# Performance work log

Measured on AMD Instinct MI355X. Metric: run time of the kernel, lower is better.

The kernel has to match this reference:

```python
import jax, jax.numpy as jnp
import numpy as np

B, C, O, H, W, K = 8, 64, 64, 96, 96, 3
PAD = 1


def setup_inputs() -> dict:
    key = jax.random.key(0)
    ks = jax.random.split(key, 5)
    x = jax.random.normal(ks[0], (B, C, H, W), jnp.float32)
    # small offset weights so sampled offsets stay O(1) pixel, like a trained net
    offset_w = jax.random.normal(ks[1], (2 * K * K, C, K, K), jnp.float32) * 0.01
    offset_b = jnp.zeros((2 * K * K,), jnp.float32)
    conv_w = jax.random.normal(ks[2], (O, C, K, K), jnp.float32) * (1.0 / np.sqrt(C * K * K))
    conv_b = jax.random.normal(ks[3], (O,), jnp.float32) * 0.01
    return {"x": x, "offset_w": offset_w, "offset_b": offset_b,
            "conv_w": conv_w, "conv_b": conv_b}


def _conv2d(x, w, b, pad):
    out = jax.lax.conv_general_dilated(
        x, w, window_strides=(1, 1), padding=[(pad, pad), (pad, pad)],
        dimension_numbers=("NCHW", "OIHW", "NCHW"))
    return out + b[None, :, None, None]


def _gather(x_flat, yi, xi):
    # x_flat: [B, C, H*W]; yi, xi: [B, K2, H, W] int32 sample indices
    valid = (yi >= 0) & (yi < H) & (xi >= 0) & (xi < W)
    idx = jnp.clip(yi, 0, H - 1) * W + jnp.clip(xi, 0, W - 1)
    idx_f = idx.reshape(idx.shape[0], -1)  # [B, K2*H*W]
    vals = jax.vmap(lambda xf, i: xf[:, i])(x_flat, idx_f)  # [B, C, K2*H*W]
    vals = vals.reshape(x_flat.shape[0], x_flat.shape[1], *idx.shape[1:])
    return vals * valid[:, None].astype(vals.dtype)  # zero padding outside


def _deform_conv2d(x, offset, w, b, pad):
    # Faithful to torchvision.ops.deform_conv2d (v1, 1 offset group, stride 1)
    K2 = K * K
    off = offset.reshape(offset.shape[0], K2, 2, H, W)
    dy, dx = off[:, :, 0], off[:, :, 1]  # (dy, dx) per kernel tap, torchvision order
    ky = jnp.repeat(jnp.arange(K), K).astype(x.dtype)  # row index i of tap k=i*K+j
    kx = jnp.tile(jnp.arange(K), K).astype(x.dtype)    # col index j
    # fractional sample positions [B, K2, H, W]
    py = jnp.arange(H, dtype=x.dtype)[None, None, :, None] - pad + ky[None, :, None, None] + dy
    px = jnp.arange(W, dtype=x.dtype)[None, None, None, :] - pad + kx[None, :, None, None] + dx
    y0 = jnp.floor(py)
    x0 = jnp.floor(px)
    wy = (py - y0)[:, None]  # broadcast over channels
    wx = (px - x0)[:, None]
    y0i = y0.astype(jnp.int32)
    x0i = x0.astype(jnp.int32)
    x_flat = x.reshape(x.shape[0], x.shape[1], H * W)
    g00 = _gather(x_flat, y0i, x0i)
    g01 = _gather(x_flat, y0i, x0i + 1)
    g10 = _gather(x_flat, y0i + 1, x0i)
    g11 = _gather(x_flat, y0i + 1, x0i + 1)
    # bilinear interp -> sampled patches [B, C, K2, H, W]
    sampled = (g00 * (1 - wy) * (1 - wx) + g01 * (1 - wy) * wx
               + g10 * wy * (1 - wx) + g11 * wy * wx)
    out = jnp.einsum("bckhw,ock->bohw", sampled, w.reshape(w.shape[0], w.shape[1], K2))
    return out + b[None, :, None, None]


def reference(x, offset_w, offset_b, conv_w, conv_b):
    offset = _conv2d(x, offset_w, offset_b, PAD)  # [B, 18, H, W]
    return _deform_conv2d(x, offset, conv_w, conv_b, PAD)
```

## Files before the change

kernel.cpp:

```cpp
#include <hip/hip_runtime.h>

#define Bb 8
#define Cc 64
#define Oo 64
#define Hh 96
#define Ww 96
#define HW 9216
#define NOFF 18

typedef __bf16 bf16_t;
typedef __bf16 bf16x2 __attribute__((ext_vector_type(2)));
typedef __bf16 bf16x8 __attribute__((ext_vector_type(8)));
typedef float  f32x4  __attribute__((ext_vector_type(4)));

#define OFFS_SZ (Bb*NOFF*HW)
#define XT_SZ   (Bb*HW*Cc)
#define WTPD_SZ (18*4*64*8)
#define WTPO_SZ (18*2*64*8)

__global__ void xpose_kernel(const float* __restrict__ x, bf16_t* __restrict__ xt) {
    __shared__ float tile[64][65];
    int bid  = blockIdx.x;
    int b    = bid / 144;
    int t0   = (bid % 144) * 64;
    int lane = threadIdx.x & 63;
    int sub  = threadIdx.x >> 6;
    const float* xb = x + (size_t)b * Cc * HW;
    #pragma unroll
    for (int i = 0; i < 16; ++i) {
        int c = sub * 16 + i;
        tile[c][lane] = xb[c * HW + t0 + lane];
    }
    __syncthreads();
    bf16_t* xtb = xt + ((size_t)b * HW + t0) * Cc;
    int half = lane >> 5, cpair = lane & 31;
    #pragma unroll
    for (int i = 0; i < 8; ++i) {
        int hw = sub * 16 + half * 8 + i;
        bf16x2 v;
        v[0] = (bf16_t)tile[cpair * 2][hw];
        v[1] = (bf16_t)tile[cpair * 2 + 1][hw];
        *(bf16x2*)&xtb[hw * Cc + cpair * 2] = v;
    }
}

__global__ void prep_w(const float* __restrict__ cw, const float* __restrict__ ow,
                       bf16_t* __restrict__ wtpd, bf16_t* __restrict__ wtpo) {
    if (blockIdx.x < 18) {
        int n = blockIdx.x * 256 + threadIdx.x;
        int t = n >> 8; int rem = n & 255; int mt = rem >> 6; int l = rem & 63;
        int o = mt * 16 + (l & 15);
        int kbase = t * 32 + ((l >> 4) & 3) * 8;
        bf16x8 v;
        #pragma unroll
        for (int j = 0; j < 8; ++j) {
            int kidx = kbase + j; int k = kidx >> 6; int c = kidx & 63;
            v[j] = (bf16_t)cw[(o * 64 + c) * 9 + k];
        }
        *(bf16x8*)&wtpd[n * 8] = v;
    } else {
        int n = (blockIdx.x - 18) * 256 + threadIdx.x;
        int t = n >> 7; int rem = n & 127; int mt = rem >> 6; int l = rem & 63;
        int oc = mt * 16 + (l & 15);
        int kbase = t * 32 + ((l >> 4) & 3) * 8;
        bf16x8 v;
        #pragma unroll
        for (int j = 0; j < 8; ++j) {
            int kidx = kbase + j; int k = kidx >> 6; int c = kidx & 63;
            v[j] = (oc < NOFF) ? (bf16_t)ow[(oc * 64 + c) * 9 + k] : (bf16_t)0.f;
        }
        *(bf16x8*)&wtpo[n * 8] = v;
    }
}


__global__ __launch_bounds__(256, 4) void offconv_mfma(const bf16_t* __restrict__ xt,
        const bf16_t* __restrict__ wtpo, const float* __restrict__ ob,
        float* __restrict__ offs) {
    __shared__ bf16_t Sb[4][16 * 72];
    int bid = blockIdx.x;
    int b = bid & 7, hw0 = (bid >> 3) * 64;
    int tid = threadIdx.x, lane = tid & 63, q = tid >> 6;
    int cg = lane & 7, prow = lane >> 3;
    int cb8 = cg * 8;
    int ph[2], pw[2];
    #pragma unroll
    for (int i = 0; i < 2; ++i) {
        int hw = hw0 + q * 16 + i * 8 + prow;
        ph[i] = hw / 96; pw[i] = hw % 96;
    }
    f32x4 acc[2];
    #pragma unroll
    for (int mt = 0; mt < 2; ++mt)
        #pragma unroll
        for (int r = 0; r < 4; ++r) {
            int oc = mt * 16 + ((lane >> 4) & 3) * 4 + r;
            acc[mt][r] = (oc < NOFF) ? ob[oc] : 0.f;
        }
    bf16_t* myS = &Sb[q][0];
    int bbase = b * HW;

    bf16x8 g[2];
    auto issue = [&](int k, bf16x8 (&gg)[2]) {
        const int ky = k / 3, kx = k % 3;
        #pragma unroll
        for (int i = 0; i < 2; ++i) {
            int y = ph[i] - 1 + ky, x = pw[i] - 1 + kx;
            bool valid = (y >= 0) && (y < Hh) && (x >= 0) && (x < Ww);
            bf16x8 v;
            #pragma unroll
            for (int j = 0; j < 8; ++j) v[j] = (bf16_t)0.f;
            if (valid) v = *(const bf16x8*)(xt + ((bbase + y * Ww + x) * Cc + cb8));
            gg[i] = v;
        }
    };
    issue(0, g);
    #pragma unroll
    for (int k = 0; k < 9; ++k) {
        #pragma unroll
        for (int i = 0; i < 2; ++i)
            *(bf16x8*)&myS[(i * 8 + prow) * 72 + cb8] = g[i];
        if (k < 8) issue(k + 1, g);
        #pragma unroll
        for (int s = 0; s < 2; ++s) {
            bf16x8 bfrag = *(bf16x8*)&myS[(lane & 15) * 72 + s * 32 + ((lane >> 4) & 3) * 8];
            int t = k * 2 + s;
            #pragma unroll
            for (int mt = 0; mt < 2; ++mt) {
                bf16x8 afrag = *(const bf16x8*)&wtpo[((t * 2 + mt) * 64 + lane) * 8];
                acc[mt] = __builtin_amdgcn_mfma_f32_16x16x32_bf16(afrag, bfrag, acc[mt], 0, 0, 0);
            }
        }
    }
    #pragma unroll
    for (int mt = 0; mt < 2; ++mt)
        #pragma unroll
        for (int r = 0; r < 4; ++r) {
            int oc = mt * 16 + ((lane >> 4) & 3) * 4 + r;
            if (oc < NOFF)
                offs[(b * NOFF + oc) * HW + hw0 + q * 16 + (lane & 15)] = acc[mt][r];
        }
}

__global__ __launch_bounds__(256, 4) void deform_mfma(const bf16_t* __restrict__ xt,
        const float* __restrict__ offs, const bf16_t* __restrict__ wtpd,
        const float* __restrict__ cb, float* __restrict__ out) {
    __shared__ float offbuf[64 * 20];
    __shared__ bf16_t Sa[4][16 * 72];
    int bid = blockIdx.x;
    int b = bid & 7, hw0 = (bid >> 3) * 64;
    int tid = threadIdx.x, lane = tid & 63, q = tid >> 6;
    {
        int pix = tid & 63, oc0 = tid >> 6;
        #pragma unroll
        for (int r = 0; r < 5; ++r) {
            int oc = oc0 + r * 4;
            if (oc < NOFF)
                offbuf[pix * 20 + oc] = offs[(b * NOFF + oc) * HW + hw0 + pix];
        }
    }
    __syncthreads();
    int cg = lane & 7, prow = lane >> 3;
    int cb8 = cg * 8;
    int pl[2], ph[2], pw[2];
    #pragma unroll
    for (int i = 0; i < 2; ++i) {
        pl[i] = q * 16 + i * 8 + prow;
        int hw = hw0 + pl[i];
        ph[i] = hw / 96; pw[i] = hw % 96;
    }
    f32x4 acc[4];
    #pragma unroll
    for (int mt = 0; mt < 4; ++mt)
        #pragma unroll
        for (int r = 0; r < 4; ++r)
            acc[mt][r] = cb[mt * 16 + ((lane >> 4) & 3) * 4 + r];
    bf16_t* myS = &Sa[q][0];
    int bbase = b * HW;

    bf16x8 g[2][4];
    float w4[2][4];
    auto issue = [&](int k, bf16x8 (&gg)[2][4], float (&ww)[2][4]) {
        const int ky = k / 3, kx = k % 3;
        #pragma unroll
        for (int i = 0; i < 2; ++i) {
            float2 od = *(float2*)&offbuf[pl[i] * 20 + 2 * k];
            float py = (float)(ph[i] - 1 + ky) + od.x;
            float px = (float)(pw[i] - 1 + kx) + od.y;
            float fy = floorf(py), fx = floorf(px);
            float wy = py - fy, wx = px - fx;
            int y0 = (int)fy, x0 = (int)fx;
            int y1 = y0 + 1, x1 = x0 + 1;
            bool vy0 = (unsigned)y0 < (unsigned)Hh, vy1 = (unsigned)y1 < (unsigned)Hh;
            bool vx0 = (unsigned)x0 < (unsigned)Ww, vx1 = (unsigned)x1 < (unsigned)Ww;
            int y0c = min(max(y0, 0), Hh - 1), y1c = min(max(y1, 0), Hh - 1);
            int x0c = min(max(x0, 0), Ww - 1), x1c = min(max(x1, 0), Ww - 1);
            ww[i][0] = (vy0 && vx0) ? (1.f - wy) * (1.f - wx) : 0.f;
            ww[i][1] = (vy0 && vx1) ? (1.f - wy) * wx : 0.f;
            ww[i][2] = (vy1 && vx0) ? wy * (1.f - wx) : 0.f;
            ww[i][3] = (vy1 && vx1) ? wy * wx : 0.f;
            int r0 = (bbase + y0c * Ww) * Cc, r1 = (bbase + y1c * Ww) * Cc;
            gg[i][0] = *(const bf16x8*)(xt + r0 + x0c * Cc + cb8);
            gg[i][1] = *(const bf16x8*)(xt + r0 + x1c * Cc + cb8);
            gg[i][2] = *(const bf16x8*)(xt + r1 + x0c * Cc + cb8);
            gg[i][3] = *(const bf16x8*)(xt + r1 + x1c * Cc + cb8);
        }
    };
    issue(0, g, w4);
    #pragma unroll
    for (int k = 0; k < 9; ++k) {
        #pragma unroll
        for (int i = 0; i < 2; ++i) {
            bf16x8 v;
            #pragma unroll
            for (int j = 0; j < 8; ++j) {
                float s = (float)g[i][0][j] * w4[i][0] + (float)g[i][1][j] * w4[i][1]
                        + (float)g[i][2][j] * w4[i][2] + (float)g[i][3][j] * w4[i][3];
                v[j] = (bf16_t)s;
            }
            *(bf16x8*)&myS[(i * 8 + prow) * 72 + cb8] = v;
        }
        if (k < 8) issue(k + 1, g, w4);
        #pragma unroll
        for (int s = 0; s < 2; ++s) {
            bf16x8 bfrag = *(bf16x8*)&myS[(lane & 15) * 72 + s * 32 + ((lane >> 4) & 3) * 8];
            int t = k * 2 + s;
            #pragma unroll
            for (int mt = 0; mt < 4; ++mt) {
                bf16x8 afrag = *(const bf16x8*)&wtpd[((t * 4 + mt) * 64 + lane) * 8];
                acc[mt] = __builtin_amdgcn_mfma_f32_16x16x32_bf16(afrag, bfrag, acc[mt], 0, 0, 0);
            }
        }
    }
    #pragma unroll
    for (int mt = 0; mt < 4; ++mt)
        #pragma unroll
        for (int r = 0; r < 4; ++r) {
            int o = mt * 16 + ((lane >> 4) & 3) * 4 + r;
            out[(b * Oo + o) * HW + hw0 + q * 16 + (lane & 15)] = acc[mt][r];
        }
}

extern "C" void kernel_launch(void* const* d_in, const int* in_sizes, int n_in,
                              void* d_out, int out_size, void* d_ws, size_t ws_size,
                              hipStream_t stream) {
    const float* x  = (const float*)d_in[0];
    const float* ow = (const float*)d_in[1];
    const float* ob = (const float*)d_in[2];
    const float* cw = (const float*)d_in[3];
    const float* cb = (const float*)d_in[4];
    float* out = (float*)d_out;

    float*  offs = (float*)d_ws;
    bf16_t* xt   = (bf16_t*)(offs + OFFS_SZ);
    bf16_t* wtpd = xt + XT_SZ;
    bf16_t* wtpo = wtpd + WTPD_SZ;

    xpose_kernel<<<1152, 256, 0, stream>>>(x, xt);
    prep_w      <<<27,   256, 0, stream>>>(cw, ow, wtpd, wtpo);
    offconv_mfma<<<1152, 256, 0, stream>>>(xt, wtpo, ob, offs);
    deform_mfma <<<1152, 256, 0, stream>>>(xt, offs, wtpd, cb, out);
}
```

Baseline: 119.9 us.

## Fuse offset conv into deform kernel and merge transpose with weight prep

Computes the offset convolution inside the deformable conv kernel and writes offsets straight to shared memory. This removes the global offset buffer round trip and one launch. The transpose and weight-prep kernels are also merged into one launch with block-index dispatch. In exchange, each block now runs both phases back to back, with a __syncthreads between them and higher per-block register and latency pressure.

Measured after the change: 113.9 us. 5.0% less time.

```diff
diff --git a/kernel.cpp b/kernel.cpp
--- a/kernel.cpp
+++ b/kernel.cpp
@@ -13,41 +13,39 @@
 typedef __bf16 bf16x8 __attribute__((ext_vector_type(8)));
 typedef float  f32x4  __attribute__((ext_vector_type(4)));
 
-#define OFFS_SZ (Bb*NOFF*HW)
 #define XT_SZ   (Bb*HW*Cc)
 #define WTPD_SZ (18*4*64*8)
 #define WTPO_SZ (18*2*64*8)
 
-__global__ void xpose_kernel(const float* __restrict__ x, bf16_t* __restrict__ xt) {
+__global__ void xpose_prep(const float* __restrict__ x, const float* __restrict__ cw,
+                           const float* __restrict__ ow, bf16_t* __restrict__ xt,
+                           bf16_t* __restrict__ wtpd, bf16_t* __restrict__ wtpo) {
     __shared__ float tile[64][65];
-    int bid  = blockIdx.x;
-    int b    = bid / 144;
-    int t0   = (bid % 144) * 64;
-    int lane = threadIdx.x & 63;
-    int sub  = threadIdx.x >> 6;
-    const float* xb = x + (size_t)b * Cc * HW;
-    #pragma unroll
-    for (int i = 0; i < 16; ++i) {
-        int c = sub * 16 + i;
-        tile[c][lane] = xb[c * HW + t0 + lane];
-    }
-    __syncthreads();
-    bf16_t* xtb = xt + ((size_t)b * HW + t0) * Cc;
-    int half = lane >> 5, cpair = lane & 31;
-    #pragma unroll
-    for (int i = 0; i < 8; ++i) {
-        int hw = sub * 16 + half * 8 + i;
-        bf16x2 v;
-        v[0] = (bf16_t)tile[cpair * 2][hw];
-        v[1] = (bf16_t)tile[cpair * 2 + 1][hw];
-        *(bf16x2*)&xtb[hw * Cc + cpair * 2] = v;
-    }
-}
-
-__global__ void prep_w(const float* __restrict__ cw, const float* __restrict__ ow,
-                       bf16_t* __restrict__ wtpd, bf16_t* __restrict__ wtpo) {
-    if (blockIdx.x < 18) {
-        int n = blockIdx.x * 256 + threadIdx.x;
+    int bid = blockIdx.x;
+    if (bid < 1152) {
+        int b    = bid / 144;
+        int t0   = (bid % 144) * 64;
+        int lane = threadIdx.x & 63;
+        int sub  = threadIdx.x >> 6;
+        const float* xb = x + (size_t)b * Cc * HW;
+        #pragma unroll
+        for (int i = 0; i < 16; ++i) {
+            int c = sub * 16 + i;
+            tile[c][lane] = xb[c * HW + t0 + lane];
+        }
+        __syncthreads();
+        bf16_t* xtb = xt + ((size_t)b * HW + t0) * Cc;
+        int half = lane >> 5, cpair = lane & 31;
+        #pragma unroll
+        for (int i = 0; i < 8; ++i) {
+            int hw = sub * 16 + half * 8 + i;
+            bf16x2 v;
+            v[0] = (bf16_t)tile[cpair * 2][hw];
+            v[1] = (bf16_t)tile[cpair * 2 + 1][hw];
+            *(bf16x2*)&xtb[hw * Cc + cpair * 2] = v;
+        }
+    } else if (bid < 1170) {
+        int n = (bid - 1152) * 256 + threadIdx.x;
         int t = n >> 8; int rem = n & 255; int mt = rem >> 6; int l = rem & 63;
         int o = mt * 16 + (l & 15);
         int kbase = t * 32 + ((l >> 4) & 3) * 8;
@@ -59,7 +57,7 @@
         }
         *(bf16x8*)&wtpd[n * 8] = v;
     } else {
-        int n = (blockIdx.x - 18) * 256 + threadIdx.x;
+        int n = (bid - 1170) * 256 + threadIdx.x;
         int t = n >> 7; int rem = n & 127; int mt = rem >> 6; int l = rem & 63;
         int oc = mt * 16 + (l & 15);
         int kbase = t * 32 + ((l >> 4) & 3) * 8;
@@ -73,95 +71,21 @@
     }
 }
 
-
-__global__ __launch_bounds__(256, 4) void offconv_mfma(const bf16_t* __restrict__ xt,
-        const bf16_t* __restrict__ wtpo, const float* __restrict__ ob,
-        float* __restrict__ offs) {
-    __shared__ bf16_t Sb[4][16 * 72];
+__global__ __launch_bounds__(256, 4) void fused_dcn(const bf16_t* __restrict__ xt,
+        const bf16_t* __restrict__ wtpo, const bf16_t* __restrict__ wtpd,
+        const float* __restrict__ ob, const float* __restrict__ cb,
+        float* __restrict__ out) {
+    __shared__ float offbuf[64 * 20];
+    __shared__ bf16_t Sa[4][16 * 72];
+
     int bid = blockIdx.x;
     int b = bid & 7, hw0 = (bid >> 3) * 64;
     int tid = threadIdx.x, lane = tid & 63, q = tid >> 6;
     int cg = lane & 7, prow = lane >> 3;
     int cb8 = cg * 8;
-    int ph[2], pw[2];
-    #pragma unroll
-    for (int i = 0; i < 2; ++i) {
-        int hw = hw0 + q * 16 + i * 8 + prow;
-        ph[i] = hw / 96; pw[i] = hw % 96;
-    }
-    f32x4 acc[2];
-    #pragma unroll
-    for (int mt = 0; mt < 2; ++mt)
-        #pragma unroll
-        for (int r = 0; r < 4; ++r) {
-            int oc = mt * 16 + ((lane >> 4) & 3) * 4 + r;
-            acc[mt][r] = (oc < NOFF) ? ob[oc] : 0.f;
-        }
-    bf16_t* myS = &Sb[q][0];
+    bf16_t* myS = &Sa[q][0];
     int bbase = b * HW;
 
-    bf16x8 g[2];
-    auto issue = [&](int k, bf16x8 (&gg)[2]) {
-        const int ky = k / 3, kx = k % 3;
-        #pragma unroll
-        for (int i = 0; i < 2; ++i) {
-            int y = ph[i] - 1 + ky, x = pw[i] - 1 + kx;
-            bool valid = (y >= 0) && (y < Hh) && (x >= 0) && (x < Ww);
-            bf16x8 v;
-            #pragma unroll
-            for (int j = 0; j < 8; ++j) v[j] = (bf16_t)0.f;
-            if (valid) v = *(const bf16x8*)(xt + ((bbase + y * Ww + x) * Cc + cb8));
-            gg[i] = v;
-        }
-    };
-    issue(0, g);
-    #pragma unroll
-    for (int k = 0; k < 9; ++k) {
-        #pragma unroll
-        for (int i = 0; i < 2; ++i)
-            *(bf16x8*)&myS[(i * 8 + prow) * 72 + cb8] = g[i];
-        if (k < 8) issue(k + 1, g);
-        #pragma unroll
-        for (int s = 0; s < 2; ++s) {
-            bf16x8 bfrag = *(bf16x8*)&myS[(lane & 15) * 72 + s * 32 + ((lane >> 4) & 3) * 8];
-            int t = k * 2 + s;
-            #pragma unroll
-            for (int mt = 0; mt < 2; ++mt) {
-                bf16x8 afrag = *(const bf16x8*)&wtpo[((t * 2 + mt) * 64 + lane) * 8];
-                acc[mt] = __builtin_amdgcn_mfma_f32_16x16x32_bf16(afrag, bfrag, acc[mt], 0, 0, 0);
-            }
-        }
-    }
-    #pragma unroll
-    for (int mt = 0; mt < 2; ++mt)
-        #pragma unroll
-        for (int r = 0; r < 4; ++r) {
-            int oc = mt * 16 + ((lane >> 4) & 3) * 4 + r;
-            if (oc < NOFF)
-                offs[(b * NOFF + oc) * HW + hw0 + q * 16 + (lane & 15)] = acc[mt][r];
-        }
-}
-
-__global__ __launch_bounds__(256, 4) void deform_mfma(const bf16_t* __restrict__ xt,
-        const float* __restrict__ offs, const bf16_t* __restrict__ wtpd,
-        const float* __restrict__ cb, float* __restrict__ out) {
-    __shared__ float offbuf[64 * 20];
-    __shared__ bf16_t Sa[4][16 * 72];
-    int bid = blockIdx.x;
-    int b = bid & 7, hw0 = (bid >> 3) * 64;
-    int tid = threadIdx.x, lane = tid & 63, q = tid >> 6;
-    {
-        int pix = tid & 63, oc0 = tid >> 6;
-        #pragma unroll
-        for (int r = 0; r < 5; ++r) {
-            int oc = oc0 + r * 4;
-            if (oc < NOFF)
-                offbuf[pix * 20 + oc] = offs[(b * NOFF + oc) * HW + hw0 + pix];
-        }
-    }
-    __syncthreads();
-    int cg = lane & 7, prow = lane >> 3;
-    int cb8 = cg * 8;
     int pl[2], ph[2], pw[2];
     #pragma unroll
     for (int i = 0; i < 2; ++i) {
@@ -169,14 +93,65 @@
         int hw = hw0 + pl[i];
         ph[i] = hw / 96; pw[i] = hw % 96;
     }
+
+    {
+        f32x4 acc[2];
+        #pragma unroll
+        for (int mt = 0; mt < 2; ++mt)
+            #pragma unroll
+            for (int r = 0; r < 4; ++r) {
+                int oc = mt * 16 + ((lane >> 4) & 3) * 4 + r;
+                acc[mt][r] = (oc < NOFF) ? ob[oc] : 0.f;
+            }
+        bf16x8 g[2];
+        auto issue = [&](int k, bf16x8 (&gg)[2]) {
+            const int ky = k / 3, kx = k % 3;
+            #pragma unroll
+            for (int i = 0; i < 2; ++i) {
+                int y = ph[i] - 1 + ky, x = pw[i] - 1 + kx;
+                bool valid = (y >= 0) && (y < Hh) && (x >= 0) && (x < Ww);
+                bf16x8 v;
+                #pragma unroll
+                for (int j = 0; j < 8; ++j) v[j] = (bf16_t)0.f;
+                if (valid) v = *(const bf16x8*)(xt + ((bbase + y * Ww + x) * Cc + cb8));
+                gg[i] = v;
+            }
+        };
+        issue(0, g);
+        #pragma unroll
+        for (int k = 0; k < 9; ++k) {
+            #pragma unroll
+            for (int i = 0; i < 2; ++i)
+                *(bf16x8*)&myS[(i * 8 + prow) * 72 + cb8] = g[i];
+            if (k < 8) issue(k + 1, g);
+            #pragma unroll
+            for (int s = 0; s < 2; ++s) {
+                bf16x8 bfrag = *(bf16x8*)&myS[(lane & 15) * 72 + s * 32 + ((lane >> 4) & 3) * 8];
+                int t = k * 2 + s;
+                #pragma unroll
+                for (int mt = 0; mt < 2; ++mt) {
+                    bf16x8 afrag = *(const bf16x8*)&wtpo[((t * 2 + mt) * 64 + lane) * 8];
+                    acc[mt] = __builtin_amdgcn_mfma_f32_16x16x32_bf16(afrag, bfrag, acc[mt], 0, 0, 0);
+                }
+            }
+        }
+        #pragma unroll
+        for (int mt = 0; mt < 2; ++mt)
+            #pragma unroll
+            for (int r = 0; r < 4; ++r) {
+                int oc = mt * 16 + ((lane >> 4) & 3) * 4 + r;
+                if (oc < NOFF)
+                    offbuf[(q * 16 + (lane & 15)) * 20 + oc] = acc[mt][r];
+            }
+    }
+    __syncthreads();
+
     f32x4 acc[4];
     #pragma unroll
     for (int mt = 0; mt < 4; ++mt)
         #pragma unroll
         for (int r = 0; r < 4; ++r)
             acc[mt][r] = cb[mt * 16 + ((lane >> 4) & 3) * 4 + r];
-    bf16_t* myS = &Sa[q][0];
-    int bbase = b * HW;
 
     bf16x8 g[2][4];
     float w4[2][4];
@@ -251,13 +226,10 @@
     const float* cb = (const float*)d_in[4];
     float* out = (float*)d_out;
 
-    float*  offs = (float*)d_ws;
-    bf16_t* xt   = (bf16_t*)(offs + OFFS_SZ);
+    bf16_t* xt   = (bf16_t*)d_ws;
     bf16_t* wtpd = xt + XT_SZ;
     bf16_t* wtpo = wtpd + WTPD_SZ;
 
-    xpose_kernel<<<1152, 256, 0, stream>>>(x, xt);
-    prep_w      <<<27,   256, 0, stream>>>(cw, ow, wtpd, wtpo);
-    offconv_mfma<<<1152, 256, 0, stream>>>(xt, wtpo, ob, offs);
-    deform_mfma <<<1152, 256, 0, stream>>>(xt, offs, wtpd, cb, out);
+    xpose_prep<<<1179, 256, 0, stream>>>(x, cw, ow, xt, wtpd, wtpo);
+    fused_dcn <<<1152, 256, 0, stream>>>(xt, wtpo, wtpd, ob, cb, out);
 }
```
